# Optimization experiments

Measured on AMD Instinct MI355X. Metric: run time of the kernel, lower is better.

The kernel has to match this reference:

```python
import jax, jax.numpy as jnp
import numpy as np

D = 1024
H = 16
HD = D // H
B = 2
T = 2048


def _rope_tables(t, hd):
    inv_freq = 1.0 / (10000.0 ** (np.arange(0, hd, 2, dtype=np.float32) / hd))
    ang = np.arange(t, dtype=np.float32)[:, None] * inv_freq[None, :]  # [T, hd/2]
    emb = np.concatenate([ang, ang], axis=-1)  # [T, hd]
    return jnp.asarray(np.cos(emb)), jnp.asarray(np.sin(emb))


def setup_inputs() -> dict:
    key = jax.random.key(0)
    kx, kq, kk, kv, ko = jax.random.split(key, 5)
    scale = 0.02
    x = jax.random.normal(kx, (B, T, D), dtype=jnp.float32)
    cos, sin = _rope_tables(T, HD)
    mask = jnp.tril(jnp.ones((T, T), dtype=jnp.int32))[None, None]  # [1,1,T,T]
    wq = jax.random.normal(kq, (D, D), dtype=jnp.float32) * scale
    wk = jax.random.normal(kk, (D, D), dtype=jnp.float32) * scale
    wv = jax.random.normal(kv, (D, D), dtype=jnp.float32) * scale
    wo = jax.random.normal(ko, (D, D), dtype=jnp.float32) * scale
    return {"x": x, "cos": cos, "sin": sin, "mask": mask,
            "wq": wq, "wk": wk, "wv": wv, "wo": wo}


def _rotate_half(t):
    t1, t2 = jnp.split(t, 2, axis=-1)
    return jnp.concatenate((-t2, t1), axis=-1)


def reference(x, cos, sin, mask, wq, wk, wv, wo):
    Bx, Tx, C = x.shape
    hd = C // H
    # nn.Linear: y = x @ W.T  -> [B,T,H,hd] -> [B,H,T,hd]
    q = (x @ wq.T).reshape(Bx, Tx, H, hd).transpose(0, 2, 1, 3)
    k = (x @ wk.T).reshape(Bx, Tx, H, hd).transpose(0, 2, 1, 3)
    v = (x @ wv.T).reshape(Bx, Tx, H, hd).transpose(0, 2, 1, 3)
    c = cos[:Tx][None, None]  # [1,1,T,hd]
    s = sin[:Tx][None, None]
    q = q * c + _rotate_half(q) * s
    k = k * c + _rotate_half(k) * s
    att = jnp.einsum('bhqd,bhkd->bhqk', q, k) * (hd ** -0.5)
    att = jnp.where(mask[:, :, :Tx, :Tx] == 0, -jnp.inf, att)
    att = jax.nn.softmax(att, axis=-1)
    out = jnp.einsum('bhqk,bhkd->bhqd', att, v)
    out = out.transpose(0, 2, 1, 3).reshape(Bx, Tx, C)
    return out @ wo.T
```

## Files before the change

### kernel.cpp

```cpp
#include <hip/hip_runtime.h>
#include <math.h>

constexpr int D  = 1024;
constexpr int H  = 16;
constexpr int HD = 64;
constexpr int B  = 2;
constexpr int T  = 2048;
constexpr int M  = B * T;

constexpr size_t XSZ = (size_t)M * D;
constexpr size_t WSZ = (size_t)D * D;

typedef float  f32x4  __attribute__((ext_vector_type(4)));
typedef __bf16 bf16x8 __attribute__((ext_vector_type(8)));
typedef __bf16 bf16x4 __attribute__((ext_vector_type(4)));

static __device__ inline f32x4 mfma16(bf16x8 a, bf16x8 b, f32x4 c) {
  return __builtin_amdgcn_mfma_f32_16x16x32_bf16(a, b, c, 0, 0, 0);
}

static __device__ inline void gload16(const __bf16* g, __bf16* l) {
  __builtin_amdgcn_global_load_lds(
      (const __attribute__((address_space(1))) void*)g,
      (__attribute__((address_space(3))) void*)l, 16, 0, 0);
}

__global__ __launch_bounds__(256)
void cvt_all(const float* __restrict__ x, const float* __restrict__ wq,
             const float* __restrict__ wk, const float* __restrict__ wv,
             const float* __restrict__ wo, __bf16* __restrict__ out) {
  size_t idx = ((size_t)blockIdx.x * 256 + threadIdx.x) * 8;
  const float* src;
  if      (idx < XSZ)            src = x  + idx;
  else if (idx < XSZ + WSZ)      src = wq + (idx - XSZ);
  else if (idx < XSZ + 2 * WSZ)  src = wk + (idx - XSZ - WSZ);
  else if (idx < XSZ + 3 * WSZ)  src = wv + (idx - XSZ - 2 * WSZ);
  else                           src = wo + (idx - XSZ - 3 * WSZ);
  float4 a = *reinterpret_cast<const float4*>(src);
  float4 b = *reinterpret_cast<const float4*>(src + 4);
  bf16x8 o;
  o[0] = (__bf16)a.x; o[1] = (__bf16)a.y; o[2] = (__bf16)a.z; o[3] = (__bf16)a.w;
  o[4] = (__bf16)b.x; o[5] = (__bf16)b.y; o[6] = (__bf16)b.z; o[7] = (__bf16)b.w;
  *reinterpret_cast<bf16x8*>(out + idx) = o;
}

template<int MODE>
__global__ __launch_bounds__(512)
void gemm_mfma(const __bf16* __restrict__ A,
               const __bf16* __restrict__ W0, const __bf16* __restrict__ W1,
               const __bf16* __restrict__ W2,
               const float* __restrict__ cosT, const float* __restrict__ sinT,
               void* __restrict__ out0, void* __restrict__ out1,
               void* __restrict__ out2) {
  __shared__ __bf16 As[128 * 64];
  __shared__ __bf16 Bs[128 * 64];

  const int tid  = threadIdx.x;
  const int lane = tid & 63;
  const int w    = tid >> 6;
  const int wm   = w >> 1;
  const int wn   = w & 1;
  const int l15  = lane & 15, lg = lane >> 4;
  const int m0   = blockIdx.y * 128;

  int which, n0;
  const __bf16* Bw;
  if (MODE == 1) {
    which = blockIdx.x >> 3;
    n0 = (blockIdx.x & 7) * 128;
    Bw = which == 0 ? W0 : which == 1 ? W1 : W2;
  } else {
    which = 0;
    n0 = blockIdx.x * 128;
    Bw = W0;
  }

  f32x4 acc[2][4];
  #pragma unroll
  for (int i = 0; i < 2; ++i)
    #pragma unroll
    for (int j = 0; j < 4; ++j) acc[i][j] = (f32x4){0.f, 0.f, 0.f, 0.f};

  const int e0 = tid * 8;
  const int r0 = e0 >> 6;
  const int c0 = e0 & 63;

  for (int k0 = 0; k0 < 1024; k0 += 64) {
    const __bf16* ga = A  + (size_t)(m0 + r0) * 1024 + k0 + c0;
    const __bf16* gb = Bw + (size_t)(n0 + r0) * 1024 + k0 + c0;
    gload16(ga,             As + e0);
    gload16(ga + 64 * 1024, As + e0 + 4096);
    gload16(gb,             Bs + e0);
    gload16(gb + 64 * 1024, Bs + e0 + 4096);
    __syncthreads();

    #pragma unroll
    for (int ks = 0; ks < 2; ++ks) {
      bf16x8 af[2], bfr[4];
      #pragma unroll
      for (int mt = 0; mt < 2; ++mt)
        af[mt] = *reinterpret_cast<const bf16x8*>(
            &As[(wm * 32 + mt * 16 + l15) * 64 + ks * 32 + lg * 8]);
      #pragma unroll
      for (int nt = 0; nt < 4; ++nt)
        bfr[nt] = *reinterpret_cast<const bf16x8*>(
            &Bs[(wn * 64 + nt * 16 + l15) * 64 + ks * 32 + lg * 8]);
      #pragma unroll
      for (int mt = 0; mt < 2; ++mt)
        #pragma unroll
        for (int nt = 0; nt < 4; ++nt)
          acc[mt][nt] = mfma16(af[mt], bfr[nt], acc[mt][nt]);
    }
    __syncthreads();
  }

  if (MODE == 0) {
    float* o = (float*)out0;
    #pragma unroll
    for (int mt = 0; mt < 2; ++mt) {
      const int mb = m0 + wm * 32 + mt * 16 + lg * 4;
      #pragma unroll
      for (int nt = 0; nt < 4; ++nt) {
        const int n = n0 + wn * 64 + nt * 16 + l15;
        #pragma unroll
        for (int r = 0; r < 4; ++r)
          o[(size_t)(mb + r) * 1024 + n] = acc[mt][nt][r];
      }
    }
  } else if (which < 2) {
    __bf16* dst = which == 0 ? (__bf16*)out0 : (__bf16*)out1;
    const int h = (n0 + wn * 64) >> 6;
    #pragma unroll
    for (int mt = 0; mt < 2; ++mt) {
      const int tb   = m0 + wm * 32 + mt * 16 + lg * 4;
      const int bb   = tb >> 11;
      const int tloc = tb & 2047;
      #pragma unroll
      for (int r = 0; r < 4; ++r) {
        const int t = tloc + r;
        #pragma unroll
        for (int nt = 0; nt < 2; ++nt) {
          const int hd = nt * 16 + l15;
          const float c = cosT[t * HD + hd];
          const float s = sinT[t * HD + hd];
          const float v1 = acc[mt][nt][r];
          const float v2 = acc[mt][nt + 2][r];
          const size_t base = (((size_t)(bb * H + h)) * T + t) * HD;
          dst[base + hd]      = (__bf16)(v1 * c - v2 * s);
          dst[base + hd + 32] = (__bf16)(v2 * c + v1 * s);
        }
      }
    }
  } else {
    __bf16* dst = (__bf16*)out2;
    const int h = (n0 + wn * 64) >> 6;
    #pragma unroll
    for (int mt = 0; mt < 2; ++mt) {
      const int tb = m0 + wm * 32 + mt * 16 + lg * 4;
      const int bb = tb >> 11;
      const int t0 = tb & 2047;
      #pragma unroll
      for (int nt = 0; nt < 4; ++nt) {
        const int hd = nt * 16 + l15;
        bf16x4 ov;
        #pragma unroll
        for (int r = 0; r < 4; ++r) ov[r] = (__bf16)acc[mt][nt][r];
        *reinterpret_cast<bf16x4*>(
            &dst[(((size_t)(bb * H + h)) * HD + hd) * T + t0]) = ov;
      }
    }
  }
}

__global__ __launch_bounds__(256)
void attn_v3(const __bf16* __restrict__ Q, const __bf16* __restrict__ K,
             const __bf16* __restrict__ Vt, __bf16* __restrict__ Ob) {
  __shared__ __bf16 Kl[2][64 * 64];
  __shared__ __bf16 Vl[2][64 * 64];
  __shared__ __bf16 Ps[4][32][72];

  const int tid  = threadIdx.x;
  const int lane = tid & 63;
  const int w    = tid >> 6;
  const int l15  = lane & 15, lg = lane >> 4;
  const int pair = blockIdx.x;
  const int bh   = blockIdx.y;

  const __bf16* Qg = Q  + (size_t)bh * T * HD;
  const __bf16* Kg = K  + (size_t)bh * T * HD;
  const __bf16* Vg = Vt + (size_t)bh * HD * T;

  const int r0a = tid >> 3,        c0a = tid & 7;
  const int r0b = (tid + 256) >> 3, c0b = tid & 7;
  const int cda = c0a ^ (r0a & 7);
  const int cdb = c0b ^ (r0b & 7);

  auto STAGE = [&](int kb, int buf) {
    const int j0 = kb * 64;
    gload16(Kg + (size_t)(j0 + r0a) * HD + cda * 8, &Kl[buf][tid * 8]);
    gload16(Kg + (size_t)(j0 + r0b) * HD + cdb * 8, &Kl[buf][(tid + 256) * 8]);
    gload16(Vg + (size_t)r0a * T + j0 + cda * 8,    &Vl[buf][tid * 8]);
    gload16(Vg + (size_t)r0b * T + j0 + cdb * 8,    &Vl[buf][(tid + 256) * 8]);
  };

  auto process_job = [&](int qbase) {
    const int q0 = qbase + w * 32;
    bf16x8 qf[2][2];
    #pragma unroll
    for (int qg = 0; qg < 2; ++qg) {
      const int qa = q0 + qg * 16 + l15;
      qf[qg][0] = *reinterpret_cast<const bf16x8*>(Qg + (size_t)qa * HD + lg * 8);
      qf[qg][1] = *reinterpret_cast<const bf16x8*>(Qg + (size_t)qa * HD + 32 + lg * 8);
    }

    float m_run[2] = {-INFINITY, -INFINITY};
    float l_run[2] = {0.f, 0.f};
    f32x4 oacc[2][4];
    #pragma unroll
    for (int qg = 0; qg < 2; ++qg)
      #pragma unroll
      for (int dt = 0; dt < 4; ++dt) oacc[qg][dt] = (f32x4){0.f, 0.f, 0.f, 0.f};

    const int nkb = qbase / 64 + 2;
    STAGE(0, 0);

    #pragma unroll 1
    for (int kb = 0; kb < nkb; ++kb) {
      const int cur = kb & 1;
      if (kb + 1 < nkb) {
        STAGE(kb + 1, cur ^ 1);
        asm volatile("s_waitcnt vmcnt(4)" ::: "memory");
      } else {
        asm volatile("s_waitcnt vmcnt(0)" ::: "memory");
      }
      __builtin_amdgcn_s_barrier();
      __builtin_amdgcn_sched_barrier(0);

      const int j0 = kb * 64;
      f32x4 sa[2][4];
      #pragma unroll
      for (int qg = 0; qg < 2; ++qg)
        #pragma unroll
        for (int kt = 0; kt < 4; ++kt) sa[qg][kt] = (f32x4){0.f, 0.f, 0.f, 0.f};
      #pragma unroll
      for (int ks = 0; ks < 2; ++ks) {
        bf16x8 kf[4];
        #pragma unroll
        for (int kt = 0; kt < 4; ++kt) {
          const int row = kt * 16 + l15;
          const int c   = ks * 4 + lg;
          kf[kt] = *reinterpret_cast<const bf16x8*>(
              &Kl[cur][row * 64 + ((c ^ (row & 7)) << 3)]);
        }
        #pragma unroll
        for (int qg = 0; qg < 2; ++qg)
          #pragma unroll
          for (int kt = 0; kt < 4; ++kt)
            sa[qg][kt] = mfma16(kf[kt], qf[qg][ks], sa[qg][kt]);
      }

      #pragma unroll
      for (int qg = 0; qg < 2; ++qg) {
        const int q_abs = q0 + qg * 16 + l15;
        const bool diag = (j0 + 63 > q0 + qg * 16);
        float p[16];
        float smax = -INFINITY;
        #pragma unroll
        for (int kt = 0; kt < 4; ++kt)
          #pragma unroll
          for (int r = 0; r < 4; ++r) {
            float s = sa[qg][kt][r] * 0.125f;
            if (diag && (j0 + kt * 16 + lg * 4 + r) > q_abs) s = -INFINITY;
            p[kt * 4 + r] = s;
            smax = fmaxf(smax, s);
          }
        smax = fmaxf(smax, __shfl_xor(smax, 16));
        smax = fmaxf(smax, __shfl_xor(smax, 32));
        const float m_new = fmaxf(m_run[qg], smax);
        const float resc  = __expf(m_run[qg] - m_new);
        float psum = 0.f;
        #pragma unroll
        for (int i = 0; i < 16; ++i) {
          float e = __expf(p[i] - m_new);
          p[i] = e;
          psum += e;
        }
        psum += __shfl_xor(psum, 16);
        psum += __shfl_xor(psum, 32);
        l_run[qg] = l_run[qg] * resc + psum;
        m_run[qg] = m_new;
        #pragma unroll
        for (int dt = 0; dt < 4; ++dt) oacc[qg][dt] *= resc;

        #pragma unroll
        for (int kt = 0; kt < 4; ++kt) {
          bf16x4 pk;
          #pragma unroll
          for (int r = 0; r < 4; ++r) pk[r] = (__bf16)p[kt * 4 + r];
          *reinterpret_cast<bf16x4*>(&Ps[w][qg * 16 + l15][kt * 16 + lg * 4]) = pk;
        }
      }

      #pragma unroll
      for (int ks = 0; ks < 2; ++ks) {
        bf16x8 pf[2];
        #pragma unroll
        for (int qg = 0; qg < 2; ++qg)
          pf[qg] = *reinterpret_cast<const bf16x8*>(
              &Ps[w][qg * 16 + l15][ks * 32 + lg * 8]);
        #pragma unroll
        for (int dt = 0; dt < 4; ++dt) {
          const int row = dt * 16 + l15;
          const int c   = ks * 4 + lg;
          bf16x8 vf = *reinterpret_cast<const bf16x8*>(
              &Vl[cur][row * 64 + ((c ^ (row & 7)) << 3)]);
          #pragma unroll
          for (int qg = 0; qg < 2; ++qg)
            oacc[qg][dt] = mfma16(vf, pf[qg], oacc[qg][dt]);
        }
      }

      __builtin_amdgcn_sched_barrier(0);
      __builtin_amdgcn_s_barrier();
    }

    const int b = bh >> 4, h = bh & 15;
    #pragma unroll
    for (int qg = 0; qg < 2; ++qg) {
      const int q_abs = q0 + qg * 16 + l15;
      const float inv = 1.f / l_run[qg];
      const size_t rowbase = ((size_t)(b * T + q_abs)) * 1024 + h * 64;
      #pragma unroll
      for (int dt = 0; dt < 4; ++dt) {
        bf16x4 o;
        #pragma unroll
        for (int r = 0; r < 4; ++r) o[r] = (__bf16)(oacc[qg][dt][r] * inv);
        *reinterpret_cast<bf16x4*>(&Ob[rowbase + dt * 16 + lg * 4]) = o;
      }
    }
  };

  process_job(pair * 128);
  process_job((15 - pair) * 128);
}

extern "C" void kernel_launch(void* const* d_in, const int* in_sizes, int n_in,
                              void* d_out, int out_size, void* d_ws, size_t ws_size,
                              hipStream_t stream) {
  const float* x    = (const float*)d_in[0];
  const float* cosT = (const float*)d_in[1];
  const float* sinT = (const float*)d_in[2];
  const float* wq   = (const float*)d_in[4];
  const float* wk   = (const float*)d_in[5];
  const float* wv   = (const float*)d_in[6];
  const float* wo   = (const float*)d_in[7];
  float* out = (float*)d_out;

  __bf16* xb   = (__bf16*)d_ws;
  __bf16* wqb  = xb  + XSZ;
  __bf16* wkb  = wqb + WSZ;
  __bf16* wvb  = wkb + WSZ;
  __bf16* wob  = wvb + WSZ;
  __bf16* Qh   = wob + WSZ;
  __bf16* Kh   = Qh  + XSZ;
  __bf16* Vth  = Kh  + XSZ;
  __bf16* attb = Vth + XSZ;

  cvt_all<<<(XSZ + 4 * WSZ) / 8 / 256, 256, 0, stream>>>(x, wq, wk, wv, wo, xb);

  gemm_mfma<1><<<dim3(24, 32), 512, 0, stream>>>(
      xb, wqb, wkb, wvb, cosT, sinT, Qh, Kh, Vth);

  attn_v3<<<dim3(8, 32), 256, 0, stream>>>(Qh, Kh, Vth, attb);

  gemm_mfma<0><<<dim3(8, 32), 512, 0, stream>>>(
      attb, wob, nullptr, nullptr, nullptr, nullptr, out, nullptr, nullptr);
}
```

Measured before the change: 156.8 us.

## Launch one query tile per block, heaviest first, with exp2 softmax and setprio

The attention kernel no longer pairs a light and a heavy query tile in each block. It now launches 16x32 blocks, each handling one 128-query tile, in reverse order so the longest causal tiles start first. This doubles the block count to 512 to improve occupancy and tail balance on the many CUs, at the cost of a less even per-block workload. It also folds log2(e) into the scale and uses exp2f, shrinks the padding of the P buffer in LDS, and raises wave priority around the PV MFMA section.

```diff
diff --git a/kernel.cpp b/kernel.cpp
--- a/kernel.cpp
+++ b/kernel.cpp
@@ -173,175 +173,177 @@
 }
 
 __global__ __launch_bounds__(256)
-void attn_v3(const __bf16* __restrict__ Q, const __bf16* __restrict__ K,
+void attn_v5(const __bf16* __restrict__ Q, const __bf16* __restrict__ K,
              const __bf16* __restrict__ Vt, __bf16* __restrict__ Ob) {
   __shared__ __bf16 Kl[2][64 * 64];
   __shared__ __bf16 Vl[2][64 * 64];
-  __shared__ __bf16 Ps[4][32][72];
+  __shared__ __bf16 Ps[4][32][68];
 
   const int tid  = threadIdx.x;
   const int lane = tid & 63;
   const int w    = tid >> 6;
   const int l15  = lane & 15, lg = lane >> 4;
-  const int pair = blockIdx.x;
+  const int qb   = 15 - (int)blockIdx.x;
   const int bh   = blockIdx.y;
+  const int qbase = qb * 128;
+  const int q0    = qbase + w * 32;
 
   const __bf16* Qg = Q  + (size_t)bh * T * HD;
   const __bf16* Kg = K  + (size_t)bh * T * HD;
   const __bf16* Vg = Vt + (size_t)bh * HD * T;
 
-  const int r0a = tid >> 3,        c0a = tid & 7;
-  const int r0b = (tid + 256) >> 3, c0b = tid & 7;
-  const int cda = c0a ^ (r0a & 7);
-  const int cdb = c0b ^ (r0b & 7);
-
-  auto STAGE = [&](int kb, int buf) {
+  const int r0a = tid >> 3;
+  const int r0b = r0a + 32;
+  const int c0  = tid & 7;
+  const int cda = c0 ^ (r0a & 7);
+
+#define STAGE(kb_, buf_)                                                      \
+  do {                                                                        \
+    const int _j0 = (kb_) * 64;                                               \
+    gload16(Kg + (size_t)(_j0 + r0a) * HD + cda * 8, &Kl[buf_][tid * 8]);     \
+    gload16(Kg + (size_t)(_j0 + r0b) * HD + cda * 8, &Kl[buf_][(tid + 256) * 8]); \
+    gload16(Vg + (size_t)r0a * T + _j0 + cda * 8,    &Vl[buf_][tid * 8]);     \
+    gload16(Vg + (size_t)r0b * T + _j0 + cda * 8,    &Vl[buf_][(tid + 256) * 8]); \
+  } while (0)
+
+  bf16x8 qf[2][2];
+  #pragma unroll
+  for (int qg = 0; qg < 2; ++qg) {
+    const int qa = q0 + qg * 16 + l15;
+    qf[qg][0] = *reinterpret_cast<const bf16x8*>(Qg + (size_t)qa * HD + lg * 8);
+    qf[qg][1] = *reinterpret_cast<const bf16x8*>(Qg + (size_t)qa * HD + 32 + lg * 8);
+  }
+
+  float m_run[2] = {-INFINITY, -INFINITY};
+  float l_run[2] = {0.f, 0.f};
+  f32x4 oacc[2][4];
+  #pragma unroll
+  for (int qg = 0; qg < 2; ++qg)
+    #pragma unroll
+    for (int dt = 0; dt < 4; ++dt) oacc[qg][dt] = (f32x4){0.f, 0.f, 0.f, 0.f};
+
+  const int nkb = 2 * qb + 2;
+  STAGE(0, 0);
+
+  const float SCALE = 0.125f * 1.44269504f;
+
+  #pragma unroll 1
+  for (int kb = 0; kb < nkb; ++kb) {
+    const int cur = kb & 1;
+    if (kb + 1 < nkb) {
+      STAGE(kb + 1, cur ^ 1);
+      asm volatile("s_waitcnt vmcnt(4)" ::: "memory");
+    } else {
+      asm volatile("s_waitcnt vmcnt(0)" ::: "memory");
+    }
+    __builtin_amdgcn_s_barrier();
+    __builtin_amdgcn_sched_barrier(0);
+
     const int j0 = kb * 64;
-    gload16(Kg + (size_t)(j0 + r0a) * HD + cda * 8, &Kl[buf][tid * 8]);
-    gload16(Kg + (size_t)(j0 + r0b) * HD + cdb * 8, &Kl[buf][(tid + 256) * 8]);
-    gload16(Vg + (size_t)r0a * T + j0 + cda * 8,    &Vl[buf][tid * 8]);
-    gload16(Vg + (size_t)r0b * T + j0 + cdb * 8,    &Vl[buf][(tid + 256) * 8]);
-  };
-
-  auto process_job = [&](int qbase) {
-    const int q0 = qbase + w * 32;
-    bf16x8 qf[2][2];
-    #pragma unroll
-    for (int qg = 0; qg < 2; ++qg) {
-      const int qa = q0 + qg * 16 + l15;
-      qf[qg][0] = *reinterpret_cast<const bf16x8*>(Qg + (size_t)qa * HD + lg * 8);
-      qf[qg][1] = *reinterpret_cast<const bf16x8*>(Qg + (size_t)qa * HD + 32 + lg * 8);
-    }
-
-    float m_run[2] = {-INFINITY, -INFINITY};
-    float l_run[2] = {0.f, 0.f};
-    f32x4 oacc[2][4];
+    f32x4 sa[2][4];
     #pragma unroll
     for (int qg = 0; qg < 2; ++qg)
       #pragma unroll
-      for (int dt = 0; dt < 4; ++dt) oacc[qg][dt] = (f32x4){0.f, 0.f, 0.f, 0.f};
-
-    const int nkb = qbase / 64 + 2;
-    STAGE(0, 0);
-
-    #pragma unroll 1
-    for (int kb = 0; kb < nkb; ++kb) {
-      const int cur = kb & 1;
-      if (kb + 1 < nkb) {
-        STAGE(kb + 1, cur ^ 1);
-        asm volatile("s_waitcnt vmcnt(4)" ::: "memory");
-      } else {
-        asm volatile("s_waitcnt vmcnt(0)" ::: "memory");
-      }
-      __builtin_amdgcn_s_barrier();
-      __builtin_amdgcn_sched_barrier(0);
-
-      const int j0 = kb * 64;
-      f32x4 sa[2][4];
+      for (int kt = 0; kt < 4; ++kt) sa[qg][kt] = (f32x4){0.f, 0.f, 0.f, 0.f};
+    #pragma unroll
+    for (int ks = 0; ks < 2; ++ks) {
+      bf16x8 kf[4];
+      #pragma unroll
+      for (int kt = 0; kt < 4; ++kt) {
+        const int row = kt * 16 + l15;
+        const int c   = ks * 4 + lg;
+        kf[kt] = *reinterpret_cast<const bf16x8*>(
+            &Kl[cur][row * 64 + ((c ^ (row & 7)) << 3)]);
+      }
       #pragma unroll
       for (int qg = 0; qg < 2; ++qg)
         #pragma unroll
-        for (int kt = 0; kt < 4; ++kt) sa[qg][kt] = (f32x4){0.f, 0.f, 0.f, 0.f};
-      #pragma unroll
-      for (int ks = 0; ks < 2; ++ks) {
-        bf16x8 kf[4];
-        #pragma unroll
-        for (int kt = 0; kt < 4; ++kt) {
-          const int row = kt * 16 + l15;
-          const int c   = ks * 4 + lg;
-          kf[kt] = *reinterpret_cast<const bf16x8*>(
-              &Kl[cur][row * 64 + ((c ^ (row & 7)) << 3)]);
-        }
-        #pragma unroll
-        for (int qg = 0; qg < 2; ++qg)
-          #pragma unroll
-          for (int kt = 0; kt < 4; ++kt)
-            sa[qg][kt] = mfma16(kf[kt], qf[qg][ks], sa[qg][kt]);
-      }
-
-      #pragma unroll
-      for (int qg = 0; qg < 2; ++qg) {
-        const int q_abs = q0 + qg * 16 + l15;
-        const bool diag = (j0 + 63 > q0 + qg * 16);
-        float p[16];
-        float smax = -INFINITY;
-        #pragma unroll
         for (int kt = 0; kt < 4; ++kt)
-          #pragma unroll
-          for (int r = 0; r < 4; ++r) {
-            float s = sa[qg][kt][r] * 0.125f;
-            if (diag && (j0 + kt * 16 + lg * 4 + r) > q_abs) s = -INFINITY;
-            p[kt * 4 + r] = s;
-            smax = fmaxf(smax, s);
-          }
-        smax = fmaxf(smax, __shfl_xor(smax, 16));
-        smax = fmaxf(smax, __shfl_xor(smax, 32));
-        const float m_new = fmaxf(m_run[qg], smax);
-        const float resc  = __expf(m_run[qg] - m_new);
-        float psum = 0.f;
-        #pragma unroll
-        for (int i = 0; i < 16; ++i) {
-          float e = __expf(p[i] - m_new);
-          p[i] = e;
-          psum += e;
-        }
-        psum += __shfl_xor(psum, 16);
-        psum += __shfl_xor(psum, 32);
-        l_run[qg] = l_run[qg] * resc + psum;
-        m_run[qg] = m_new;
-        #pragma unroll
-        for (int dt = 0; dt < 4; ++dt) oacc[qg][dt] *= resc;
-
-        #pragma unroll
-        for (int kt = 0; kt < 4; ++kt) {
-          bf16x4 pk;
-          #pragma unroll
-          for (int r = 0; r < 4; ++r) pk[r] = (__bf16)p[kt * 4 + r];
-          *reinterpret_cast<bf16x4*>(&Ps[w][qg * 16 + l15][kt * 16 + lg * 4]) = pk;
-        }
-      }
-
-      #pragma unroll
-      for (int ks = 0; ks < 2; ++ks) {
-        bf16x8 pf[2];
-        #pragma unroll
-        for (int qg = 0; qg < 2; ++qg)
-          pf[qg] = *reinterpret_cast<const bf16x8*>(
-              &Ps[w][qg * 16 + l15][ks * 32 + lg * 8]);
-        #pragma unroll
-        for (int dt = 0; dt < 4; ++dt) {
-          const int row = dt * 16 + l15;
-          const int c   = ks * 4 + lg;
-          bf16x8 vf = *reinterpret_cast<const bf16x8*>(
-              &Vl[cur][row * 64 + ((c ^ (row & 7)) << 3)]);
-          #pragma unroll
-          for (int qg = 0; qg < 2; ++qg)
-            oacc[qg][dt] = mfma16(vf, pf[qg], oacc[qg][dt]);
-        }
-      }
-
-      __builtin_amdgcn_sched_barrier(0);
-      __builtin_amdgcn_s_barrier();
-    }
-
-    const int b = bh >> 4, h = bh & 15;
+          sa[qg][kt] = mfma16(kf[kt], qf[qg][ks], sa[qg][kt]);
+    }
+
     #pragma unroll
     for (int qg = 0; qg < 2; ++qg) {
       const int q_abs = q0 + qg * 16 + l15;
-      const float inv = 1.f / l_run[qg];
-      const size_t rowbase = ((size_t)(b * T + q_abs)) * 1024 + h * 64;
+      const bool diag = (j0 + 63 > q0 + qg * 16);
+      float p[16];
+      float smax = -INFINITY;
+      #pragma unroll
+      for (int kt = 0; kt < 4; ++kt)
+        #pragma unroll
+        for (int r = 0; r < 4; ++r) {
+          float s = sa[qg][kt][r] * SCALE;
+          if (diag && (j0 + kt * 16 + lg * 4 + r) > q_abs) s = -INFINITY;
+          p[kt * 4 + r] = s;
+          smax = fmaxf(smax, s);
+        }
+      smax = fmaxf(smax, __shfl_xor(smax, 16));
+      smax = fmaxf(smax, __shfl_xor(smax, 32));
+      const float m_new = fmaxf(m_run[qg], smax);
+      const float resc  = exp2f(m_run[qg] - m_new);
+      float psum = 0.f;
+      #pragma unroll
+      for (int i = 0; i < 16; ++i) {
+        float e = exp2f(p[i] - m_new);
+        p[i] = e;
+        psum += e;
+      }
+      psum += __shfl_xor(psum, 16);
+      psum += __shfl_xor(psum, 32);
+      l_run[qg] = l_run[qg] * resc + psum;
+      m_run[qg] = m_new;
+      #pragma unroll
+      for (int dt = 0; dt < 4; ++dt) oacc[qg][dt] *= resc;
+
+      #pragma unroll
+      for (int kt = 0; kt < 4; ++kt) {
+        bf16x4 pk;
+        #pragma unroll
+        for (int r = 0; r < 4; ++r) pk[r] = (__bf16)p[kt * 4 + r];
+        *reinterpret_cast<bf16x4*>(&Ps[w][qg * 16 + l15][kt * 16 + lg * 4]) = pk;
+      }
+    }
+
+    __builtin_amdgcn_s_setprio(1);
+    #pragma unroll
+    for (int ks = 0; ks < 2; ++ks) {
+      bf16x8 pf[2];
+      #pragma unroll
+      for (int qg = 0; qg < 2; ++qg)
+        pf[qg] = *reinterpret_cast<const bf16x8*>(
+            &Ps[w][qg * 16 + l15][ks * 32 + lg * 8]);
       #pragma unroll
       for (int dt = 0; dt < 4; ++dt) {
-        bf16x4 o;
-        #pragma unroll
-        for (int r = 0; r < 4; ++r) o[r] = (__bf16)(oacc[qg][dt][r] * inv);
-        *reinterpret_cast<bf16x4*>(&Ob[rowbase + dt * 16 + lg * 4]) = o;
-      }
-    }
-  };
-
-  process_job(pair * 128);
-  process_job((15 - pair) * 128);
+        const int row = dt * 16 + l15;
+        const int c   = ks * 4 + lg;
+        bf16x8 vf = *reinterpret_cast<const bf16x8*>(
+            &Vl[cur][row * 64 + ((c ^ (row & 7)) << 3)]);
+        #pragma unroll
+        for (int qg = 0; qg < 2; ++qg)
+          oacc[qg][dt] = mfma16(vf, pf[qg], oacc[qg][dt]);
+      }
+    }
+    __builtin_amdgcn_s_setprio(0);
+
+    __builtin_amdgcn_sched_barrier(0);
+    __builtin_amdgcn_s_barrier();
+  }
+#undef STAGE
+
+  const int b = bh >> 4, h = bh & 15;
+  #pragma unroll
+  for (int qg = 0; qg < 2; ++qg) {
+    const int q_abs = q0 + qg * 16 + l15;
+    const float inv = 1.f / l_run[qg];
+    const size_t rowbase = ((size_t)(b * T + q_abs)) * 1024 + h * 64;
+    #pragma unroll
+    for (int dt = 0; dt < 4; ++dt) {
+      bf16x4 o;
+      #pragma unroll
+      for (int r = 0; r < 4; ++r) o[r] = (__bf16)(oacc[qg][dt][r] * inv);
+      *reinterpret_cast<bf16x4*>(&Ob[rowbase + dt * 16 + lg * 4]) = o;
+    }
+  }
 }
 
 extern "C" void kernel_launch(void* const* d_in, const int* in_sizes, int n_in,
@@ -371,7 +373,7 @@
   gemm_mfma<1><<<dim3(24, 32), 512, 0, stream>>>(
       xb, wqb, wkb, wvb, cosT, sinT, Qh, Kh, Vth);
 
-  attn_v3<<<dim3(8, 32), 256, 0, stream>>>(Qh, Kh, Vth, attb);
+  attn_v5<<<dim3(16, 32), 256, 0, stream>>>(Qh, Kh, Vth, attb);
 
   gemm_mfma<0><<<dim3(8, 32), 512, 0, stream>>>(
       attb, wob, nullptr, nullptr, nullptr, nullptr, out, nullptr, nullptr);
```

New measurement: 177.6 us. 13.2% more time.
